# Kernel optimization log

Measured on AMD Instinct MI355X. Metric: run time of the kernel, lower is better.

## Reference

```python
import jax, jax.numpy as jnp
import numpy as np

NEIGHBOR_K = 3


def setup_inputs() -> dict:
    key = jax.random.key(0)
    k1, k2 = jax.random.split(key)
    x1 = jax.random.normal(k1, (64, 640, 441), dtype=jnp.float32)   # [B, C, l] queries
    x2 = jax.random.normal(k2, (32, 640, 2205), dtype=jnp.float32)  # [N, C, m] support classes
    return {"x1": x1, "x2": x2}


def reference(x1, x2):
    # x1: [B, C, l] query local descriptors; x2: [N, C, m] support-class descriptors
    q = jnp.swapaxes(x1, 1, 2)                                   # [B, l, C]
    q = q / jnp.linalg.norm(q, axis=-1, keepdims=True)           # L2-normalize each descriptor
    s = x2 / jnp.linalg.norm(x2, axis=1, keepdims=True)          # normalize each support column over C

    def per_class(sj):                                            # sj: [C, m]
        scores = jnp.einsum('blc,cm->blm', q, sj)                # [B, l, m] cosine sims
        topk_vals = jax.lax.top_k(scores, NEIGHBOR_K)[0]         # [B, l, k] top-k over support descriptors
        return jnp.sum(topk_vals, axis=(1, 2))                   # [B] image-to-class similarity

    # map over support classes to avoid materializing [B, N, l, m]
    sims = jax.lax.map(per_class, s)                              # [N, B]
    return sims.T                                                 # [B, N]
```

## Files before the change

kernel.cpp:

```cpp
#include <hip/hip_runtime.h>
#include <hip/hip_bf16.h>
#include <float.h>

#define BQ    64
#define CDIM  640
#define LQ    441
#define NCLS  32
#define MS    2205
#define ITILES 7
#define JCHUNK 256
#define NJC    9
#define NKC    10
#define NEG_INF (-3.0e38f)

#define ABYTES 81920
#define ADW    20480
#define BMC    327680
#define BN     (NJC * BMC)

typedef __attribute__((ext_vector_type(8))) short short8;
typedef __attribute__((ext_vector_type(4))) float f32x4;

__device__ __forceinline__ void ins3(float s, float& a, float& b, float& c) {
  float x0 = fmaxf(a, s), x1 = fminf(a, s);
  float y1 = fmaxf(b, x1), y2 = fminf(b, x1);
  a = x0; b = y1; c = fmaxf(c, y2);
}

__global__ __launch_bounds__(256) void prep_q(const float* __restrict__ x1,
                                              unsigned short* __restrict__ Abf) {
  const int it = blockIdx.x;
  const int b  = blockIdx.y;
  const int t  = threadIdx.x;
  const int il = t & 63, cg = t >> 6;
  __shared__ float red[4][64];
  __shared__ float rnq[64];
  __shared__ unsigned short tile[64][66];

  const int i = it * 64 + il;
  float ss = 0.f;
  if (i < LQ) {
    for (int c = cg; c < CDIM; c += 4) {
      float v = x1[((size_t)b * CDIM + c) * LQ + i];
      ss += v * v;
    }
  }
  red[cg][il] = ss;
  __syncthreads();
  if (t < 64) {
    float s = red[0][t] + red[1][t] + red[2][t] + red[3][t];
    rnq[t] = (it * 64 + t < LQ) ? rsqrtf(s) : 0.f;
  }
  __syncthreads();

  unsigned int* blob = (unsigned int*)Abf + (size_t)(b * ITILES + it) * ADW;
  for (int kc = 0; kc < NKC; ++kc) {
    for (int idx = t; idx < 4096; idx += 256) {
      int cc = idx >> 6, ii = idx & 63;
      int gi = it * 64 + ii;
      float v = 0.f;
      if (gi < LQ) v = x1[((size_t)b * CDIM + kc * 64 + cc) * LQ + gi] * rnq[ii];
      __hip_bfloat16 h = __float2bfloat16(v);
      tile[cc][ii] = *(unsigned short*)&h;
    }
    __syncthreads();
    for (int idx = t; idx < 2048; idx += 256) {
      int row = idx >> 5, kp = idx & 31;
      unsigned int lo = tile[kp * 2][row], hi = tile[kp * 2 + 1][row];
      blob[row * 320 + kc * 32 + kp] = lo | (hi << 16);
    }
    __syncthreads();
  }
}

__global__ __launch_bounds__(256) void prep_s(const float* __restrict__ x2,
                                              char* __restrict__ Bbf) {
  const int mc = blockIdx.x;
  const int n  = blockIdx.y;
  const int t  = threadIdx.x;
  __shared__ float rns[256];
  __shared__ unsigned short tile[64][266];

  const int j = mc * 256 + t;
  float ss = 0.f;
  if (j < MS) {
    for (int c = 0; c < CDIM; ++c) {
      float v = x2[((size_t)n * CDIM + c) * MS + j];
      ss += v * v;
    }
  }
  rns[t] = (j < MS) ? rsqrtf(ss) : 0.f;
  __syncthreads();

  char* blob = Bbf + ((size_t)n * NJC + mc) * BMC;
  for (int kc = 0; kc < NKC; ++kc) {
    for (int idx = t; idx < 16384; idx += 256) {
      int cc = idx >> 8, jj = idx & 255;
      int gj = mc * 256 + jj;
      float v = 0.f;
      if (gj < MS) v = x2[((size_t)n * CDIM + kc * 64 + cc) * MS + gj] * rns[jj];
      __hip_bfloat16 h = __float2bfloat16(v);
      tile[cc][jj] = *(unsigned short*)&h;
    }
    __syncthreads();
    for (int g = t; g < 2048; g += 256) {
      int ks = g >> 10, jf = (g >> 6) & 15, ln = g & 63;
      int qq = ln >> 4, cl = ln & 15;
      int col = jf * 16 + cl, k0 = ks * 32 + qq * 8;
      unsigned int u0 = (unsigned int)tile[k0 + 0][col] | ((unsigned int)tile[k0 + 1][col] << 16);
      unsigned int u1 = (unsigned int)tile[k0 + 2][col] | ((unsigned int)tile[k0 + 3][col] << 16);
      unsigned int u2 = (unsigned int)tile[k0 + 4][col] | ((unsigned int)tile[k0 + 5][col] << 16);
      unsigned int u3 = (unsigned int)tile[k0 + 6][col] | ((unsigned int)tile[k0 + 7][col] << 16);
      int4 w; w.x = u0; w.y = u1; w.z = u2; w.w = u3;
      *(int4*)(blob + (size_t)kc * 32768 + (size_t)g * 16) = w;
    }
    __syncthreads();
  }
}

__global__ __launch_bounds__(256, 2) void gemm_topk(const int4* __restrict__ Abf,
                                                    const char* __restrict__ Bbf,
                                                    float* __restrict__ out) {
  const int bid = blockIdx.x;
  const int xcd = bid & 7;
  const int s   = bid >> 3;
  const int n   = xcd * 4 + s / 448;
  const int bx  = s % 448;
  const int b   = bx / 7;
  const int t    = threadIdx.x;
  const int lane = t & 63, wave = t >> 6;
  const int l15  = lane & 15, q = lane >> 4;

  __shared__ __align__(16) char smem[ABYTES];

  {
    const int4* gA = Abf + (size_t)bx * 5120;
    int4* sA = (int4*)smem;
    #pragma unroll
    for (int rep = 0; rep < 20; ++rep) {
      int g0 = t + rep * 256;
      int i = g0 / 80;
      int g = g0 - i * 80;
      sA[i * 80 + (g ^ (i & 7))] = gA[g0];
    }
  }
  __syncthreads();

  float t3[16][3];
  #pragma unroll
  for (int r = 0; r < 16; ++r) { t3[r][0] = NEG_INF; t3[r][1] = NEG_INF; t3[r][2] = NEG_INF; }

  const int swz  = l15 & 7;
  const int oct0 = (q ^ swz) * 16;
  const int oct1 = ((4 + q) ^ swz) * 16;
  const char* Ab = smem + l15 * 1280;

  const char* BnB = Bbf + (size_t)n * BN + wave * 4096 + lane * 16;

  short8 bcur[2][4], bnxt[2][4];
  int off = 0;
  #pragma unroll
  for (int ks = 0; ks < 2; ++ks)
    #pragma unroll
    for (int c = 0; c < 4; ++c)
      bcur[ks][c] = *(const short8*)(BnB + ks * 16384 + c * 1024);

  for (int mc = 0; mc < NJC; ++mc) {
    f32x4 acc[4][4];
    #pragma unroll
    for (int r = 0; r < 4; ++r)
      #pragma unroll
      for (int c = 0; c < 4; ++c) acc[r][c] = (f32x4){0.f, 0.f, 0.f, 0.f};

    #pragma unroll 2
    for (int kc = 0; kc < NKC; ++kc) {
      int offn = off + 32768;
      if (offn == BN) offn = 0;
      #pragma unroll
      for (int ks = 0; ks < 2; ++ks)
        #pragma unroll
        for (int c = 0; c < 4; ++c)
          bnxt[ks][c] = *(const short8*)(BnB + offn + ks * 16384 + c * 1024);

      #pragma unroll
      for (int ks = 0; ks < 2; ++ks) {
        const int oct = ks ? oct1 : oct0;
        short8 af[4];
        #pragma unroll
        for (int r = 0; r < 4; ++r)
          af[r] = *(const short8*)(Ab + r * 20480 + kc * 128 + oct);
        #pragma unroll
        for (int r = 0; r < 4; ++r)
          #pragma unroll
          for (int c = 0; c < 4; ++c)
            acc[r][c] = __builtin_amdgcn_mfma_f32_16x16x32_bf16(af[r], bcur[ks][c], acc[r][c], 0, 0, 0);
      }
      #pragma unroll
      for (int ks = 0; ks < 2; ++ks)
        #pragma unroll
        for (int c = 0; c < 4; ++c) bcur[ks][c] = bnxt[ks][c];
      off = offn;
    }

    #pragma unroll
    for (int c = 0; c < 4; ++c) {
      const int jg = mc * JCHUNK + wave * 64 + c * 16 + l15;
      const bool jv = jg < MS;
      #pragma unroll
      for (int r = 0; r < 4; ++r)
        #pragma unroll
        for (int reg = 0; reg < 4; ++reg) {
          float sv = jv ? acc[r][c][reg] : NEG_INF;
          ins3(sv, t3[r * 4 + reg][0], t3[r * 4 + reg][1], t3[r * 4 + reg][2]);
        }
    }
  }

  __syncthreads();
  float* mrg = (float*)smem;
  float* aux = (float*)(smem + 49152);
  #pragma unroll
  for (int r = 0; r < 4; ++r)
    #pragma unroll
    for (int reg = 0; reg < 4; ++reg) {
      int row = r * 16 + q * 4 + reg;
      int col = wave * 16 + l15;
      float* p = &mrg[(row * 64 + col) * 3];
      p[0] = t3[r * 4 + reg][0]; p[1] = t3[r * 4 + reg][1]; p[2] = t3[r * 4 + reg][2];
    }
  __syncthreads();
  {
    int row = t >> 2, seg = t & 3;
    float a = NEG_INF, bb = NEG_INF, cc = NEG_INF;
    for (int c0 = seg * 16; c0 < seg * 16 + 16; ++c0) {
      const float* p = &mrg[(row * 64 + c0) * 3];
      ins3(p[0], a, bb, cc); ins3(p[1], a, bb, cc); ins3(p[2], a, bb, cc);
    }
    aux[(row * 4 + seg) * 3 + 0] = a;
    aux[(row * 4 + seg) * 3 + 1] = bb;
    aux[(row * 4 + seg) * 3 + 2] = cc;
  }
  __syncthreads();
  if (t < 64) {
    float a = NEG_INF, bb = NEG_INF, cc = NEG_INF;
    for (int v = 0; v < 12; ++v) ins3(aux[t * 12 + v], a, bb, cc);
    float sum = a + bb + cc;
    for (int offr = 32; offr > 0; offr >>= 1) sum += __shfl_down(sum, offr);
    if (t == 0) atomicAdd(&out[b * NCLS + n], sum);
  }
}

extern "C" void kernel_launch(void* const* d_in, const int* in_sizes, int n_in,
                              void* d_out, int out_size, void* d_ws, size_t ws_size,
                              hipStream_t stream) {
  const float* x1 = (const float*)d_in[0];
  const float* x2 = (const float*)d_in[1];
  float* out = (float*)d_out;

  unsigned short* Abf = (unsigned short*)d_ws;
  char* Bbf = (char*)d_ws + (size_t)BQ * ITILES * ABYTES;

  hipMemsetAsync(d_out, 0, BQ * NCLS * sizeof(float), stream);
  prep_q<<<dim3(ITILES, BQ), 256, 0, stream>>>(x1, Abf);
  prep_s<<<dim3(NJC, NCLS), 256, 0, stream>>>(x2, Bbf);
  gemm_topk<<<BQ * ITILES * NCLS, 256, 0, stream>>>((const int4*)Abf, Bbf, out);
}
```

Before: 3.121 ms.

## Use 12-wave blocks sharing the query tile, fragment-major A layout, med3 top-3

The GEMM+top-k kernel now launches 768-thread blocks, so 12 waves share one staged query tile and each covers 64 support columns of a 768-wide chunk, cutting the outer chunk loop from 9 to 3. The support and query blobs are re-laid out in MFMA fragment order, so LDS reads need no XOR swizzle and the A tile is copied to LDS linearly. The top-3 insertion uses fmed3, and the cross-lane merge is done with xor shuffles before a small LDS reduction. This reduces redundant A staging per block and merge overhead, at the cost of larger blocks that may limit occupancy under the 3-blocks-per-CU launch bound and possible LDS bank conflicts from dropping the swizzle.

```diff
diff --git a/kernel.cpp b/kernel.cpp
--- a/kernel.cpp
+++ b/kernel.cpp
@@ -8,27 +8,28 @@
 #define NCLS  32
 #define MS    2205
 #define ITILES 7
-#define JCHUNK 256
-#define NJC    9
+#define WCHUNK 768
+#define NJC3   3
 #define NKC    10
 #define NEG_INF (-3.0e38f)
 
 #define ABYTES 81920
-#define ADW    20480
-#define BMC    327680
-#define BN     (NJC * BMC)
+#define BKC    98304
+#define BMC3   (NKC * BKC)
+#define BN     (NJC3 * BMC3)
 
 typedef __attribute__((ext_vector_type(8))) short short8;
 typedef __attribute__((ext_vector_type(4))) float f32x4;
 
 __device__ __forceinline__ void ins3(float s, float& a, float& b, float& c) {
-  float x0 = fmaxf(a, s), x1 = fminf(a, s);
-  float y1 = fmaxf(b, x1), y2 = fminf(b, x1);
-  a = x0; b = y1; c = fmaxf(c, y2);
+  float na = fmaxf(a, s);
+  float nb = __builtin_amdgcn_fmed3f(a, b, s);
+  float nc = __builtin_amdgcn_fmed3f(b, c, s);
+  a = na; b = nb; c = nc;
 }
 
 __global__ __launch_bounds__(256) void prep_q(const float* __restrict__ x1,
-                                              unsigned short* __restrict__ Abf) {
+                                              char* __restrict__ Abf) {
   const int it = blockIdx.x;
   const int b  = blockIdx.y;
   const int t  = threadIdx.x;
@@ -53,7 +54,7 @@
   }
   __syncthreads();
 
-  unsigned int* blob = (unsigned int*)Abf + (size_t)(b * ITILES + it) * ADW;
+  int4* gblob = (int4*)(Abf + (size_t)(b * ITILES + it) * ABYTES);
   for (int kc = 0; kc < NKC; ++kc) {
     for (int idx = t; idx < 4096; idx += 256) {
       int cc = idx >> 6, ii = idx & 63;
@@ -64,10 +65,16 @@
       tile[cc][ii] = *(unsigned short*)&h;
     }
     __syncthreads();
-    for (int idx = t; idx < 2048; idx += 256) {
-      int row = idx >> 5, kp = idx & 31;
-      unsigned int lo = tile[kp * 2][row], hi = tile[kp * 2 + 1][row];
-      blob[row * 320 + kc * 32 + kp] = lo | (hi << 16);
+    for (int g = t; g < 512; g += 256) {
+      int ks = g >> 8, r = (g >> 6) & 3, ln = g & 63;
+      int q = ln >> 4, cl = ln & 15;
+      int row = r * 16 + cl, k0 = ks * 32 + q * 8;
+      unsigned int u0 = (unsigned int)tile[k0 + 0][row] | ((unsigned int)tile[k0 + 1][row] << 16);
+      unsigned int u1 = (unsigned int)tile[k0 + 2][row] | ((unsigned int)tile[k0 + 3][row] << 16);
+      unsigned int u2 = (unsigned int)tile[k0 + 4][row] | ((unsigned int)tile[k0 + 5][row] << 16);
+      unsigned int u3 = (unsigned int)tile[k0 + 6][row] | ((unsigned int)tile[k0 + 7][row] << 16);
+      int4 w; w.x = u0; w.y = u1; w.z = u2; w.w = u3;
+      gblob[kc * 512 + g] = w;
     }
     __syncthreads();
   }
@@ -75,13 +82,14 @@
 
 __global__ __launch_bounds__(256) void prep_s(const float* __restrict__ x2,
                                               char* __restrict__ Bbf) {
-  const int mc = blockIdx.x;
+  const int jc = blockIdx.x;
   const int n  = blockIdx.y;
   const int t  = threadIdx.x;
+  const int mc3 = jc / 3, jt3 = jc % 3;
   __shared__ float rns[256];
   __shared__ unsigned short tile[64][266];
 
-  const int j = mc * 256 + t;
+  const int j = jc * 256 + t;
   float ss = 0.f;
   if (j < MS) {
     for (int c = 0; c < CDIM; ++c) {
@@ -92,11 +100,11 @@
   rns[t] = (j < MS) ? rsqrtf(ss) : 0.f;
   __syncthreads();
 
-  char* blob = Bbf + ((size_t)n * NJC + mc) * BMC;
+  char* blob = Bbf + ((size_t)n * NJC3 + mc3) * BMC3;
   for (int kc = 0; kc < NKC; ++kc) {
     for (int idx = t; idx < 16384; idx += 256) {
       int cc = idx >> 8, jj = idx & 255;
-      int gj = mc * 256 + jj;
+      int gj = jc * 256 + jj;
       float v = 0.f;
       if (gj < MS) v = x2[((size_t)n * CDIM + kc * 64 + cc) * MS + gj] * rns[jj];
       __hip_bfloat16 h = __float2bfloat16(v);
@@ -112,13 +120,13 @@
       unsigned int u2 = (unsigned int)tile[k0 + 4][col] | ((unsigned int)tile[k0 + 5][col] << 16);
       unsigned int u3 = (unsigned int)tile[k0 + 6][col] | ((unsigned int)tile[k0 + 7][col] << 16);
       int4 w; w.x = u0; w.y = u1; w.z = u2; w.w = u3;
-      *(int4*)(blob + (size_t)kc * 32768 + (size_t)g * 16) = w;
-    }
-    __syncthreads();
-  }
-}
-
-__global__ __launch_bounds__(256, 2) void gemm_topk(const int4* __restrict__ Abf,
+      *(int4*)(blob + (size_t)kc * BKC + (size_t)(ks * 3072 + (jt3 * 16 + jf) * 64 + ln) * 16) = w;
+    }
+    __syncthreads();
+  }
+}
+
+__global__ __launch_bounds__(768, 3) void gemm_topk(const char* __restrict__ Abf,
                                                     const char* __restrict__ Bbf,
                                                     float* __restrict__ out) {
   const int bid = blockIdx.x;
@@ -134,15 +142,9 @@
   __shared__ __align__(16) char smem[ABYTES];
 
   {
-    const int4* gA = Abf + (size_t)bx * 5120;
+    const int4* gA = (const int4*)(Abf + (size_t)bx * ABYTES);
     int4* sA = (int4*)smem;
-    #pragma unroll
-    for (int rep = 0; rep < 20; ++rep) {
-      int g0 = t + rep * 256;
-      int i = g0 / 80;
-      int g = g0 - i * 80;
-      sA[i * 80 + (g ^ (i & 7))] = gA[g0];
-    }
+    for (int idx = t; idx < 5120; idx += 768) sA[idx] = gA[idx];
   }
   __syncthreads();
 
@@ -150,22 +152,18 @@
   #pragma unroll
   for (int r = 0; r < 16; ++r) { t3[r][0] = NEG_INF; t3[r][1] = NEG_INF; t3[r][2] = NEG_INF; }
 
-  const int swz  = l15 & 7;
-  const int oct0 = (q ^ swz) * 16;
-  const int oct1 = ((4 + q) ^ swz) * 16;
-  const char* Ab = smem + l15 * 1280;
-
   const char* BnB = Bbf + (size_t)n * BN + wave * 4096 + lane * 16;
+  const char* As  = smem + lane * 16;
 
   short8 bcur[2][4], bnxt[2][4];
-  int off = 0;
   #pragma unroll
   for (int ks = 0; ks < 2; ++ks)
     #pragma unroll
     for (int c = 0; c < 4; ++c)
-      bcur[ks][c] = *(const short8*)(BnB + ks * 16384 + c * 1024);
-
-  for (int mc = 0; mc < NJC; ++mc) {
+      bcur[ks][c] = *(const short8*)(BnB + ks * 49152 + c * 1024);
+  int off = 0;
+
+  for (int mc = 0; mc < NJC3; ++mc) {
     f32x4 acc[4][4];
     #pragma unroll
     for (int r = 0; r < 4; ++r)
@@ -174,21 +172,20 @@
 
     #pragma unroll 2
     for (int kc = 0; kc < NKC; ++kc) {
-      int offn = off + 32768;
+      int offn = off + BKC;
       if (offn == BN) offn = 0;
       #pragma unroll
       for (int ks = 0; ks < 2; ++ks)
         #pragma unroll
         for (int c = 0; c < 4; ++c)
-          bnxt[ks][c] = *(const short8*)(BnB + offn + ks * 16384 + c * 1024);
+          bnxt[ks][c] = *(const short8*)(BnB + offn + ks * 49152 + c * 1024);
 
       #pragma unroll
       for (int ks = 0; ks < 2; ++ks) {
-        const int oct = ks ? oct1 : oct0;
         short8 af[4];
         #pragma unroll
         for (int r = 0; r < 4; ++r)
-          af[r] = *(const short8*)(Ab + r * 20480 + kc * 128 + oct);
+          af[r] = *(const short8*)(As + kc * 8192 + ks * 4096 + r * 1024);
         #pragma unroll
         for (int r = 0; r < 4; ++r)
           #pragma unroll
@@ -204,7 +201,7 @@
 
     #pragma unroll
     for (int c = 0; c < 4; ++c) {
-      const int jg = mc * JCHUNK + wave * 64 + c * 16 + l15;
+      const int jg = mc * WCHUNK + wave * 64 + c * 16 + l15;
       const bool jv = jg < MS;
       #pragma unroll
       for (int r = 0; r < 4; ++r)
@@ -216,34 +213,36 @@
     }
   }
 
-  __syncthreads();
-  float* mrg = (float*)smem;
-  float* aux = (float*)(smem + 49152);
   #pragma unroll
-  for (int r = 0; r < 4; ++r)
-    #pragma unroll
-    for (int reg = 0; reg < 4; ++reg) {
-      int row = r * 16 + q * 4 + reg;
-      int col = wave * 16 + l15;
-      float* p = &mrg[(row * 64 + col) * 3];
-      p[0] = t3[r * 4 + reg][0]; p[1] = t3[r * 4 + reg][1]; p[2] = t3[r * 4 + reg][2];
-    }
-  __syncthreads();
-  {
-    int row = t >> 2, seg = t & 3;
-    float a = NEG_INF, bb = NEG_INF, cc = NEG_INF;
-    for (int c0 = seg * 16; c0 < seg * 16 + 16; ++c0) {
-      const float* p = &mrg[(row * 64 + c0) * 3];
-      ins3(p[0], a, bb, cc); ins3(p[1], a, bb, cc); ins3(p[2], a, bb, cc);
-    }
-    aux[(row * 4 + seg) * 3 + 0] = a;
-    aux[(row * 4 + seg) * 3 + 1] = bb;
-    aux[(row * 4 + seg) * 3 + 2] = cc;
+  for (int m = 1; m <= 8; m <<= 1) {
+    #pragma unroll
+    for (int ri = 0; ri < 16; ++ri) {
+      float oa = __shfl_xor(t3[ri][0], m, 64);
+      float ob = __shfl_xor(t3[ri][1], m, 64);
+      float oc = __shfl_xor(t3[ri][2], m, 64);
+      ins3(oa, t3[ri][0], t3[ri][1], t3[ri][2]);
+      ins3(ob, t3[ri][0], t3[ri][1], t3[ri][2]);
+      ins3(oc, t3[ri][0], t3[ri][1], t3[ri][2]);
+    }
+  }
+
+  __syncthreads();
+  float* aux = (float*)smem;
+  if (l15 == 0) {
+    #pragma unroll
+    for (int r = 0; r < 4; ++r)
+      #pragma unroll
+      for (int reg = 0; reg < 4; ++reg) {
+        int row = r * 16 + q * 4 + reg;
+        float* p = &aux[(row * 12 + wave) * 3];
+        p[0] = t3[r * 4 + reg][0]; p[1] = t3[r * 4 + reg][1]; p[2] = t3[r * 4 + reg][2];
+      }
   }
   __syncthreads();
   if (t < 64) {
-    float a = NEG_INF, bb = NEG_INF, cc = NEG_INF;
-    for (int v = 0; v < 12; ++v) ins3(aux[t * 12 + v], a, bb, cc);
+    const float* p = &aux[t * 36];
+    float a = p[0], bb = p[1], cc = p[2];
+    for (int v = 3; v < 36; ++v) ins3(p[v], a, bb, cc);
     float sum = a + bb + cc;
     for (int offr = 32; offr > 0; offr >>= 1) sum += __shfl_down(sum, offr);
     if (t == 0) atomicAdd(&out[b * NCLS + n], sum);
@@ -257,11 +256,11 @@
   const float* x2 = (const float*)d_in[1];
   float* out = (float*)d_out;
 
-  unsigned short* Abf = (unsigned short*)d_ws;
+  char* Abf = (char*)d_ws;
   char* Bbf = (char*)d_ws + (size_t)BQ * ITILES * ABYTES;
 
   hipMemsetAsync(d_out, 0, BQ * NCLS * sizeof(float), stream);
   prep_q<<<dim3(ITILES, BQ), 256, 0, stream>>>(x1, Abf);
-  prep_s<<<dim3(NJC, NCLS), 256, 0, stream>>>(x2, Bbf);
-  gemm_topk<<<BQ * ITILES * NCLS, 256, 0, stream>>>((const int4*)Abf, Bbf, out);
-}
+  prep_s<<<dim3(9, NCLS), 256, 0, stream>>>(x2, Bbf);
+  gemm_topk<<<BQ * ITILES * NCLS, 768, 0, stream>>>(Abf, Bbf, out);
+}
```

After: 3.371 ms. +8.0%, slower.
